# Kernel tuning notes

Measured on AMD Instinct MI355X. Metric: run time of the kernel, lower is better.

Reference implementation:

```python
import jax, jax.numpy as jnp
import numpy as np

EMBED_DIM = 1024
NUM_HEADS = 16
HEAD_DIM = EMBED_DIM // NUM_HEADS
BATCH = 4
SEQ = 1024


def setup_inputs() -> dict:
    key = jax.random.key(0)
    ks = jax.random.split(key, 9)
    s = EMBED_DIM ** -0.5
    return {
        "x": jax.random.normal(ks[0], (BATCH, SEQ, EMBED_DIM), dtype=jnp.float32),
        "Wq": jax.random.normal(ks[1], (EMBED_DIM, EMBED_DIM), dtype=jnp.float32) * s,
        "bq": jnp.zeros((EMBED_DIM,), dtype=jnp.float32),
        "Wk": jax.random.normal(ks[2], (EMBED_DIM, EMBED_DIM), dtype=jnp.float32) * s,
        "bk": jnp.zeros((EMBED_DIM,), dtype=jnp.float32),
        "Wv": jax.random.normal(ks[3], (EMBED_DIM, EMBED_DIM), dtype=jnp.float32) * s,
        "bv": jnp.zeros((EMBED_DIM,), dtype=jnp.float32),
        "Wo": jax.random.normal(ks[4], (EMBED_DIM, EMBED_DIM), dtype=jnp.float32) * s,
        "bo": jnp.zeros((EMBED_DIM,), dtype=jnp.float32),
    }


def reference(x, Wq, bq, Wk, bk, Wv, bv, Wo, bo):
    B, S, E = x.shape
    H, D = NUM_HEADS, HEAD_DIM
    scale = D ** -0.5
    # QKV projections, split heads: (B, H, S, D)
    q = (x @ Wq + bq).reshape(B, S, H, D).transpose(0, 2, 1, 3)
    k = (x @ Wk + bk).reshape(B, S, H, D).transpose(0, 2, 1, 3)
    v = (x @ Wv + bv).reshape(B, S, H, D).transpose(0, 2, 1, 3)
    # causal attention scores (B, H, S, S)
    scores = jnp.einsum("bhsd,bhtd->bhst", q, k) * scale
    causal = jnp.tril(jnp.ones((S, S), dtype=bool))
    scores = jnp.where(causal, scores, -jnp.inf)
    attn = jax.nn.softmax(scores, axis=-1)  # stable; matches max-subtract + softmax
    # dropout is identity in eval mode
    out = jnp.einsum("bhst,bhtd->bhsd", attn, v)
    out = out.transpose(0, 2, 1, 3).reshape(B, S, E)
    return out @ Wo + bo
```

## Files before the change

### kernel.cpp

```cpp
#include <hip/hip_runtime.h>
#include <hip/hip_bf16.h>


typedef short bf16x8 __attribute__((ext_vector_type(8)));
typedef float f32x4  __attribute__((ext_vector_type(4)));
typedef unsigned short u16;

#define MFMA_BF16(a,b,c) __builtin_amdgcn_mfma_f32_16x16x32_bf16((a),(b),(c),0,0,0)

#define ASYNC16(gp, lp) __builtin_amdgcn_global_load_lds( \
    (const __attribute__((address_space(1))) void*)(gp),  \
    (__attribute__((address_space(3))) void*)(lp), 16, 0, 0)

__device__ __forceinline__ u16 f2bf(float f){
  unsigned int u = __float_as_uint(f);
  u += 0x7FFFu + ((u >> 16) & 1u);
  return (u16)(u >> 16);
}

__global__ __launch_bounds__(256) void cvt_x_kernel(const float* __restrict__ x,
                                                    u16* __restrict__ xb){
  int i = blockIdx.x * 256 + threadIdx.x;
  float4 v = ((const float4*)x)[i];
  ushort4 o;
  o.x = f2bf(v.x); o.y = f2bf(v.y); o.z = f2bf(v.z); o.w = f2bf(v.w);
  ((ushort4*)xb)[i] = o;
}

__global__ __launch_bounds__(256) void wtrans_kernel(const float* __restrict__ W0,
                                                     const float* __restrict__ W1,
                                                     const float* __restrict__ W2,
                                                     const float* __restrict__ W3,
                                                     u16* __restrict__ Wt){
  __shared__ float t[32][33];
  int z = blockIdx.z;
  const float* W = (z==0) ? W0 : (z==1) ? W1 : (z==2) ? W2 : W3;
  u16* out = Wt + (size_t)z * 1048576;
  int k0 = blockIdx.x * 32, n0 = blockIdx.y * 32;
  int tx = threadIdx.x & 31, ty = threadIdx.x >> 5;
  #pragma unroll
  for (int i = 0; i < 4; ++i)
    t[ty + i*8][tx] = W[(size_t)(k0 + ty + i*8) * 1024 + n0 + tx];
  __syncthreads();
  #pragma unroll
  for (int i = 0; i < 4; ++i)
    out[(size_t)(n0 + ty + i*8) * 1024 + k0 + tx] = f2bf(t[tx][ty + i*8]);
}

__device__ __forceinline__ void gemm_loop(const u16* __restrict__ Ag,
                                          const u16* __restrict__ Bg,
                                          char (*As)[8192], char (*Bs)[8192],
                                          int m0, int n0, int tid,
                                          f32x4 acc[4][4]){
  const int l  = tid & 63;
  const int lr = l & 15, hg = l >> 4;
  const int w  = tid >> 6;
  const int wr = w >> 1, wc = w & 1;
  const int r0 = tid >> 2,          cc0 = (tid & 3) ^ ((r0 ^ (r0 >> 2)) & 3);
  const int c1 = tid + 256;
  const int r1 = c1 >> 2,           cc1 = (c1 & 3) ^ ((r1 ^ (r1 >> 2)) & 3);

  auto STAGE = [&](int kt, int b){
    const int k0 = kt * 32;
    ASYNC16(Ag + (size_t)(m0 + r0) * 1024 + k0 + cc0*8, As[b] + w*1024);
    ASYNC16(Bg + (size_t)(n0 + r0) * 1024 + k0 + cc0*8, Bs[b] + w*1024);
    ASYNC16(Ag + (size_t)(m0 + r1) * 1024 + k0 + cc1*8, As[b] + 4096 + w*1024);
    ASYNC16(Bg + (size_t)(n0 + r1) * 1024 + k0 + cc1*8, Bs[b] + 4096 + w*1024);
  };
  auto COMPUTE = [&](const char* Asb, const char* Bsb){
    bf16x8 af[4], bf[4];
    #pragma unroll
    for (int mi = 0; mi < 4; ++mi){
      int row = wr*64 + mi*16 + lr;
      af[mi] = *(const bf16x8*)(Asb + row*64 + ((hg ^ ((row ^ (row>>2)) & 3)) << 4));
    }
    #pragma unroll
    for (int ni = 0; ni < 4; ++ni){
      int row = wc*64 + ni*16 + lr;
      bf[ni] = *(const bf16x8*)(Bsb + row*64 + ((hg ^ ((row ^ (row>>2)) & 3)) << 4));
    }
    #pragma unroll
    for (int mi = 0; mi < 4; ++mi)
      #pragma unroll
      for (int ni = 0; ni < 4; ++ni)
        acc[mi][ni] = MFMA_BF16(af[mi], bf[ni], acc[mi][ni]);
  };

  STAGE(0, 0);
  __syncthreads();
  #pragma unroll 1
  for (int kt = 0; kt < 32; kt += 2){
    STAGE(kt + 1, 1);
    COMPUTE(As[0], Bs[0]);
    __syncthreads();
    if (kt + 2 < 32) STAGE(kt + 2, 0);
    COMPUTE(As[1], Bs[1]);
    __syncthreads();
  }
}

__global__ __launch_bounds__(256) void gemm_qkv_kernel(const u16* __restrict__ xb,
                                                       const u16* __restrict__ Wt,
                                                       const float* __restrict__ bq,
                                                       const float* __restrict__ bk,
                                                       const float* __restrict__ bv,
                                                       u16* __restrict__ Qb,
                                                       u16* __restrict__ Kb,
                                                       u16* __restrict__ Vt){
  __shared__ alignas(16) char As[2][8192];
  __shared__ alignas(16) char Bs[2][8192];
  const int z = blockIdx.z;
  const u16* Bg = Wt + (size_t)z * 1048576;
  const float* bias = (z==0) ? bq : (z==1) ? bk : bv;
  const int m0 = blockIdx.x * 128, n0 = blockIdx.y * 128;
  f32x4 acc[4][4];
  #pragma unroll
  for (int i = 0; i < 4; ++i)
    #pragma unroll
    for (int j = 0; j < 4; ++j)
      acc[i][j] = f32x4{0.f, 0.f, 0.f, 0.f};
  gemm_loop(xb, Bg, As, Bs, m0, n0, threadIdx.x, acc);

  const int l = threadIdx.x & 63, w = threadIdx.x >> 6;
  const int lr = l & 15, hg = l >> 4;
  const int wr = w >> 1, wc = w & 1;
  u16* outp = (z == 2) ? Vt : ((z == 1) ? Kb : Qb);
  #pragma unroll
  for (int ni = 0; ni < 4; ++ni){
    int n = n0 + wc*64 + ni*16 + lr;
    float bb = bias[n];
    int h = n >> 6, d = n & 63;
    #pragma unroll
    for (int mi = 0; mi < 4; ++mi){
      int m_base = m0 + wr*64 + mi*16 + hg*4;
      int b = m_base >> 10, s = m_base & 1023;
      if (z == 2){
        ushort4 o;
        o.x = f2bf(acc[mi][ni][0] + bb);
        o.y = f2bf(acc[mi][ni][1] + bb);
        o.z = f2bf(acc[mi][ni][2] + bb);
        o.w = f2bf(acc[mi][ni][3] + bb);
        *(ushort4*)(outp + ((size_t)((b*16 + h)*64 + d) * 1024 + s)) = o;
      } else {
        #pragma unroll
        for (int r = 0; r < 4; ++r){
          float v = acc[mi][ni][r] + bb;
          outp[(size_t)((b*16 + h)*1024 + s + r) * 64 + d] = f2bf(v);
        }
      }
    }
  }
}

__global__ __launch_bounds__(256) void attn_kernel(const u16* __restrict__ Qb,
                                                   const u16* __restrict__ Kb,
                                                   const u16* __restrict__ Vt,
                                                   u16* __restrict__ Ao){
  __shared__ alignas(16) char Ksh[2][8192];
  __shared__ alignas(16) char Vsh[2][8192];
  __shared__ alignas(16) char Ps[4 * 16 * 144];
  const int tid = threadIdx.x;
  const int l = tid & 63, w = tid >> 6;
  const int lr = l & 15, hg = l >> 4;
  const int bh = blockIdx.y;
  const u16* Qp = Qb + (size_t)bh * 65536;
  const u16* Kp = Kb + (size_t)bh * 65536;
  const u16* Vp = Vt + (size_t)bh * 65536;
  char* Pw = Ps + w * 2304;

  auto STAGE = [&](int t, int b){
    int c = tid, row = c >> 3, cc = (c & 7) ^ ((row ^ (row >> 3)) & 7);
    ASYNC16(Kp + (size_t)(t*64 + row)*64 + cc*8, Ksh[b] + w*1024);
    ASYNC16(Vp + (size_t)row*1024 + t*64 + cc*8, Vsh[b] + w*1024);
    c = tid + 256; row = c >> 3; cc = (c & 7) ^ ((row ^ (row >> 3)) & 7);
    ASYNC16(Kp + (size_t)(t*64 + row)*64 + cc*8, Ksh[b] + 4096 + w*1024);
    ASYNC16(Vp + (size_t)row*1024 + t*64 + cc*8, Vsh[b] + 4096 + w*1024);
  };

  #pragma unroll 1
  for (int pass = 0; pass < 2; ++pass){
    const int qt = (pass == 0) ? (int)blockIdx.x : 15 - (int)blockIdx.x;
    const int q0 = qt * 64;

    bf16x8 qf[2];
    {
      const u16* qrow = Qp + (size_t)(q0 + w*16 + lr) * 64 + hg*8;
      qf[0] = *(const bf16x8*)(qrow);
      qf[1] = *(const bf16x8*)(qrow + 32);
    }
    f32x4 acc[4];
    #pragma unroll
    for (int i = 0; i < 4; ++i) acc[i] = f32x4{0.f, 0.f, 0.f, 0.f};
    float mrow[4] = {-INFINITY, -INFINITY, -INFINITY, -INFINITY};
    float lrow[4] = {0.f, 0.f, 0.f, 0.f};

    STAGE(0, 0);
    __syncthreads();

    #pragma unroll 1
    for (int t = 0; t <= qt; ++t){
      const int cur = t & 1;
      if (t < qt) STAGE(t + 1, cur ^ 1);
      const char* Ks = Ksh[cur];
      const char* Vs = Vsh[cur];

      float p[4][4];
      #pragma unroll
      for (int ni = 0; ni < 4; ++ni){
        int row = ni*16 + lr;
        int s8 = (row ^ (row >> 3)) & 7;
        bf16x8 k0f = *(const bf16x8*)(Ks + row*128 + ((hg       ^ s8) << 4));
        bf16x8 k1f = *(const bf16x8*)(Ks + row*128 + (((4 + hg) ^ s8) << 4));
        f32x4 zf = f32x4{0.f, 0.f, 0.f, 0.f};
        zf = MFMA_BF16(qf[0], k0f, zf);
        zf = MFMA_BF16(qf[1], k1f, zf);
        #pragma unroll
        for (int r = 0; r < 4; ++r) p[ni][r] = zf[r] * 0.125f;
      }
      if (t == qt){
        #pragma unroll
        for (int ni = 0; ni < 4; ++ni){
          int tcol = ni*16 + lr;
          #pragma unroll
          for (int r = 0; r < 4; ++r){
            int qrow = w*16 + hg*4 + r;
            if (tcol > qrow) p[ni][r] = -INFINITY;
          }
        }
      }
      float pm[4];
      #pragma unroll
      for (int r = 0; r < 4; ++r)
        pm[r] = fmaxf(fmaxf(p[0][r], p[1][r]), fmaxf(p[2][r], p[3][r]));
      #pragma unroll
      for (int xm = 1; xm < 16; xm <<= 1)
        #pragma unroll
        for (int r = 0; r < 4; ++r)
          pm[r] = fmaxf(pm[r], __shfl_xor(pm[r], xm));
      float corr[4];
      #pragma unroll
      for (int r = 0; r < 4; ++r){
        float mn = fmaxf(mrow[r], pm[r]);
        corr[r] = __expf(mrow[r] - mn);
        mrow[r] = mn;
      }
      #pragma unroll
      for (int ni = 0; ni < 4; ++ni)
        #pragma unroll
        for (int r = 0; r < 4; ++r)
          p[ni][r] = __expf(p[ni][r] - mrow[r]);
      float psum[4];
      #pragma unroll
      for (int r = 0; r < 4; ++r)
        psum[r] = (p[0][r] + p[1][r]) + (p[2][r] + p[3][r]);
      #pragma unroll
      for (int xm = 1; xm < 16; xm <<= 1)
        #pragma unroll
        for (int r = 0; r < 4; ++r)
          psum[r] += __shfl_xor(psum[r], xm);
      #pragma unroll
      for (int r = 0; r < 4; ++r)
        lrow[r] = lrow[r] * corr[r] + psum[r];
      #pragma unroll
      for (int ni = 0; ni < 4; ++ni)
        #pragma unroll
        for (int r = 0; r < 4; ++r)
          acc[ni][r] *= corr[r];

      #pragma unroll
      for (int ni = 0; ni < 4; ++ni)
        #pragma unroll
        for (int r = 0; r < 4; ++r)
          *(u16*)(Pw + (hg*4 + r)*144 + (ni*16 + lr)*2) = f2bf(p[ni][r]);

      bf16x8 pa[2];
      pa[0] = *(const bf16x8*)(Pw + lr*144 +      hg*16);
      pa[1] = *(const bf16x8*)(Pw + lr*144 + 64 + hg*16);
      #pragma unroll
      for (int ni = 0; ni < 4; ++ni){
        int row = ni*16 + lr;
        int s8 = (row ^ (row >> 3)) & 7;
        bf16x8 v0 = *(const bf16x8*)(Vs + row*128 + ((hg       ^ s8) << 4));
        bf16x8 v1 = *(const bf16x8*)(Vs + row*128 + (((4 + hg) ^ s8) << 4));
        acc[ni] = MFMA_BF16(pa[0], v0, acc[ni]);
        acc[ni] = MFMA_BF16(pa[1], v1, acc[ni]);
      }
      __syncthreads();
    }

    const int b = bh >> 4, h = bh & 15;
    float invl[4];
    #pragma unroll
    for (int r = 0; r < 4; ++r) invl[r] = 1.f / lrow[r];
    #pragma unroll
    for (int ni = 0; ni < 4; ++ni){
      int d = ni*16 + lr;
      #pragma unroll
      for (int r = 0; r < 4; ++r){
        int q = q0 + w*16 + hg*4 + r;
        Ao[((size_t)(b*1024 + q)) * 1024 + h*64 + d] = f2bf(acc[ni][r] * invl[r]);
      }
    }
  }
}

__global__ __launch_bounds__(256) void gemm_proj_kernel(const u16* __restrict__ Ab,
                                                        const u16* __restrict__ Wot,
                                                        const float* __restrict__ bo,
                                                        float* __restrict__ out){
  __shared__ alignas(16) char As[2][8192];
  __shared__ alignas(16) char Bs[2][8192];
  const int m0 = blockIdx.x * 128, n0 = blockIdx.y * 128;
  f32x4 acc[4][4];
  #pragma unroll
  for (int i = 0; i < 4; ++i)
    #pragma unroll
    for (int j = 0; j < 4; ++j)
      acc[i][j] = f32x4{0.f, 0.f, 0.f, 0.f};
  gemm_loop(Ab, Wot, As, Bs, m0, n0, threadIdx.x, acc);

  const int l = threadIdx.x & 63, w = threadIdx.x >> 6;
  const int lr = l & 15, hg = l >> 4;
  const int wr = w >> 1, wc = w & 1;
  #pragma unroll
  for (int ni = 0; ni < 4; ++ni){
    int n = n0 + wc*64 + ni*16 + lr;
    float bb = bo[n];
    #pragma unroll
    for (int mi = 0; mi < 4; ++mi){
      #pragma unroll
      for (int r = 0; r < 4; ++r){
        int m = m0 + wr*64 + mi*16 + hg*4 + r;
        out[(size_t)m * 1024 + n] = acc[mi][ni][r] + bb;
      }
    }
  }
}

extern "C" void kernel_launch(void* const* d_in, const int* in_sizes, int n_in,
                              void* d_out, int out_size, void* d_ws, size_t ws_size,
                              hipStream_t stream){
  (void)in_sizes; (void)n_in; (void)out_size; (void)ws_size;
  const float* x  = (const float*)d_in[0];
  const float* Wq = (const float*)d_in[1];
  const float* bq = (const float*)d_in[2];
  const float* Wk = (const float*)d_in[3];
  const float* bk = (const float*)d_in[4];
  const float* Wv = (const float*)d_in[5];
  const float* bv = (const float*)d_in[6];
  const float* Wo = (const float*)d_in[7];
  const float* bo = (const float*)d_in[8];
  float* out = (float*)d_out;
  char* ws = (char*)d_ws;
  const size_t MB = 1u << 20;
  u16* xb = (u16*)(ws + 0*MB);
  u16* Wt = (u16*)(ws + 8*MB);
  u16* Qb = (u16*)(ws + 16*MB);
  u16* Kb = (u16*)(ws + 24*MB);
  u16* Vt = (u16*)(ws + 32*MB);
  u16* Ao = (u16*)(ws + 40*MB);

  cvt_x_kernel<<<4096, 256, 0, stream>>>(x, xb);
  wtrans_kernel<<<dim3(32, 32, 4), 256, 0, stream>>>(Wq, Wk, Wv, Wo, Wt);
  gemm_qkv_kernel<<<dim3(32, 8, 3), 256, 0, stream>>>(xb, Wt, bq, bk, bv, Qb, Kb, Vt);
  attn_kernel<<<dim3(8, 64), 256, 0, stream>>>(Qb, Kb, Vt, Ao);
  gemm_proj_kernel<<<dim3(32, 8), 256, 0, stream>>>(Ao, Wt + 3*1048576, bo, out);
}
```

Before: 205.1 us.

## Use partial vmcnt waits for async LDS pipelining and merge prep kernels

Replaces __syncthreads in the GEMM and attention loops with explicit s_waitcnt vmcnt(4), raw barriers and scheduling barriers, so the next tile's global-to-LDS loads can stay in flight while the current tile is computed. It also merges the x conversion and weight transpose kernels into one launch to cut launch overhead. This relies on each STAGE issuing exactly four async loads per thread. If that count is wrong the partial waits could read stale LDS.

```diff
diff --git a/kernel.cpp b/kernel.cpp
--- a/kernel.cpp
+++ b/kernel.cpp
@@ -11,6 +11,11 @@
 #define ASYNC16(gp, lp) __builtin_amdgcn_global_load_lds( \
     (const __attribute__((address_space(1))) void*)(gp),  \
     (__attribute__((address_space(3))) void*)(lp), 16, 0, 0)
+
+#define VMCNT4  asm volatile("s_waitcnt vmcnt(4)" ::: "memory")
+#define VMCNT0  asm volatile("s_waitcnt vmcnt(0)" ::: "memory")
+#define BARRIER __builtin_amdgcn_s_barrier()
+#define SCHEDB  __builtin_amdgcn_sched_barrier(0)
 
 __device__ __forceinline__ u16 f2bf(float f){
   unsigned int u = __float_as_uint(f);
@@ -18,22 +23,26 @@
   return (u16)(u >> 16);
 }
 
-__global__ __launch_bounds__(256) void cvt_x_kernel(const float* __restrict__ x,
-                                                    u16* __restrict__ xb){
-  int i = blockIdx.x * 256 + threadIdx.x;
-  float4 v = ((const float4*)x)[i];
-  ushort4 o;
-  o.x = f2bf(v.x); o.y = f2bf(v.y); o.z = f2bf(v.z); o.w = f2bf(v.w);
-  ((ushort4*)xb)[i] = o;
-}
-
-__global__ __launch_bounds__(256) void wtrans_kernel(const float* __restrict__ W0,
-                                                     const float* __restrict__ W1,
-                                                     const float* __restrict__ W2,
-                                                     const float* __restrict__ W3,
-                                                     u16* __restrict__ Wt){
+__global__ __launch_bounds__(256) void prep_kernel(const float* __restrict__ x,
+                                                   const float* __restrict__ W0,
+                                                   const float* __restrict__ W1,
+                                                   const float* __restrict__ W2,
+                                                   const float* __restrict__ W3,
+                                                   u16* __restrict__ xb,
+                                                   u16* __restrict__ Wt){
   __shared__ float t[32][33];
-  int z = blockIdx.z;
+  const int z = blockIdx.z;
+  if (z == 4){
+    int i = (blockIdx.y * 32 + blockIdx.x) * 256 + threadIdx.x;
+    #pragma unroll
+    for (int j = 0; j < 4; ++j){
+      float4 v = ((const float4*)x)[i + j * 262144];
+      ushort4 o;
+      o.x = f2bf(v.x); o.y = f2bf(v.y); o.z = f2bf(v.z); o.w = f2bf(v.w);
+      ((ushort4*)xb)[i + j * 262144] = o;
+    }
+    return;
+  }
   const float* W = (z==0) ? W0 : (z==1) ? W1 : (z==2) ? W2 : W3;
   u16* out = Wt + (size_t)z * 1048576;
   int k0 = blockIdx.x * 32, n0 = blockIdx.y * 32;
@@ -87,15 +96,17 @@
   };
 
   STAGE(0, 0);
-  __syncthreads();
+  VMCNT0; BARRIER; SCHEDB;
   #pragma unroll 1
   for (int kt = 0; kt < 32; kt += 2){
     STAGE(kt + 1, 1);
+    VMCNT4; BARRIER; SCHEDB;
     COMPUTE(As[0], Bs[0]);
-    __syncthreads();
-    if (kt + 2 < 32) STAGE(kt + 2, 0);
+    SCHEDB; BARRIER;
+    if (kt + 2 < 32){ STAGE(kt + 2, 0); VMCNT4; } else { VMCNT0; }
+    BARRIER; SCHEDB;
     COMPUTE(As[1], Bs[1]);
-    __syncthreads();
+    SCHEDB; BARRIER;
   }
 }
 
@@ -195,12 +206,14 @@
     float lrow[4] = {0.f, 0.f, 0.f, 0.f};
 
     STAGE(0, 0);
-    __syncthreads();
+    VMCNT0; BARRIER; SCHEDB;
 
     #pragma unroll 1
     for (int t = 0; t <= qt; ++t){
       const int cur = t & 1;
-      if (t < qt) STAGE(t + 1, cur ^ 1);
+      if (t < qt){ STAGE(t + 1, cur ^ 1); VMCNT4; }
+      else       { VMCNT0; }
+      BARRIER; SCHEDB;
       const char* Ks = Ksh[cur];
       const char* Vs = Vsh[cur];
 
@@ -285,7 +298,7 @@
         acc[ni] = MFMA_BF16(pa[0], v0, acc[ni]);
         acc[ni] = MFMA_BF16(pa[1], v1, acc[ni]);
       }
-      __syncthreads();
+      SCHEDB; BARRIER;
     }
 
     const int b = bh >> 4, h = bh & 15;
@@ -360,8 +373,7 @@
   u16* Vt = (u16*)(ws + 32*MB);
   u16* Ao = (u16*)(ws + 40*MB);
 
-  cvt_x_kernel<<<4096, 256, 0, stream>>>(x, xb);
-  wtrans_kernel<<<dim3(32, 32, 4), 256, 0, stream>>>(Wq, Wk, Wv, Wo, Wt);
+  prep_kernel<<<dim3(32, 32, 5), 256, 0, stream>>>(x, Wq, Wk, Wv, Wo, xb, Wt);
   gemm_qkv_kernel<<<dim3(32, 8, 3), 256, 0, stream>>>(xb, Wt, bq, bk, bv, Qb, Kb, Vt);
   attn_kernel<<<dim3(8, 64), 256, 0, stream>>>(Qb, Kb, Vt, Ao);
   gemm_proj_kernel<<<dim3(32, 8), 256, 0, stream>>>(Ao, Wt + 3*1048576, bo, out);
```

New measurement: 204.5 us. No clear change (-0.3%).
